# Kernel tuning notes

Measured on AMD Instinct MI355X. Metric: run time of the kernel, lower is better.

## Reference

```python
import jax, jax.numpy as jnp
import numpy as np

N = 100_000   # nodes
E = 3_200_000 # edges (avg degree 32)
K = 10        # propagation hops


def setup_inputs() -> dict:
    key = jax.random.key(0)
    ks = jax.random.split(key, 9)
    x = jax.random.normal(ks[0], (N, 1), dtype=jnp.float32)
    edge_index = jax.random.randint(ks[1], (2, E), 0, N, dtype=jnp.int32)
    # MLP params (lin1: 1->32, lin2: 32->64, fc2: 64->1)
    W1 = jax.random.normal(ks[2], (1, 32), dtype=jnp.float32) * 0.5
    b1 = jnp.zeros((32,), dtype=jnp.float32)
    W2 = jax.random.normal(ks[3], (32, 64), dtype=jnp.float32) * (1.0 / np.sqrt(32))
    b2 = jnp.zeros((64,), dtype=jnp.float32)
    # GPR temp coefficients, Init='Random': uniform(-b, b), b=sqrt(3/(K+1)), L1-normalized
    bound = float(np.sqrt(3.0 / (K + 1)))
    temp = jax.random.uniform(ks[4], (K + 1,), dtype=jnp.float32,
                              minval=-bound, maxval=bound)
    temp = temp / jnp.sum(jnp.abs(temp))
    W_fc = jax.random.normal(ks[5], (64, 1), dtype=jnp.float32) * (1.0 / np.sqrt(64))
    b_fc = jnp.zeros((1,), dtype=jnp.float32)
    return {"x": x, "edge_index": edge_index, "W1": W1, "b1": b1,
            "W2": W2, "b2": b2, "temp": temp, "W_fc": W_fc, "b_fc": b_fc}


def reference(x, edge_index, W1, b1, W2, b2, temp, W_fc, b_fc):
    n = x.shape[0]
    # feature MLP
    h = jax.nn.relu(x @ W1 + b1)       # [N, 32]
    h = jax.nn.relu(h @ W2 + b2)       # [N, 64]
    # gcn_norm with self-loops, edge_weight = 1
    loops = jnp.arange(n, dtype=edge_index.dtype)
    row = jnp.concatenate([edge_index[0], loops])  # source
    col = jnp.concatenate([edge_index[1], loops])  # target (aggregation index)
    ones = jnp.ones(row.shape, dtype=h.dtype)
    deg = jax.ops.segment_sum(ones, col, num_segments=n)
    dinv = jnp.where(deg > 0, jax.lax.rsqrt(deg), 0.0)
    norm = dinv[row] * dinv[col]       # [E+N]
    # K-hop GPR propagation: hidden = sum_k temp[k] * A_hat^k h
    hidden0 = temp[0] * h

    def step(carry, gamma):
        xc, hid = carry
        msg = norm[:, None] * xc[row]                       # gather + scale
        xn = jax.ops.segment_sum(msg, col, num_segments=n)  # scatter-add
        return (xn, hid + gamma * xn), None

    (_, hidden), _ = jax.lax.scan(step, (h, hidden0), temp[1:])
    return hidden @ W_fc + b_fc        # [N, 1]
```

## Files before the change

kernel.cpp:

```cpp
#include <hip/hip_runtime.h>


#define TPB  256
#define SBSH 10
#define CAP1 34304
#define EPT  16
#define CH   (TPB * EPT)

__global__ void k_zero(int* __restrict__ bcursor, int nsb) {
    int i = blockIdx.x * blockDim.x + threadIdx.x;
    if (i < nsb) bcursor[i] = 0;
}

__global__ void k_scatter(const int* __restrict__ erow, const int* __restrict__ ecol,
                          int* __restrict__ bcursor, unsigned int* __restrict__ ebuf1,
                          int e, int nsb) {
    __shared__ int hist[128];
    __shared__ int base[128];
    int t = threadIdx.x;
    int s = blockIdx.x * CH;
    int r[EPT], c[EPT];

    if (t < 128) hist[t] = 0;
    __syncthreads();
#pragma unroll
    for (int j = 0; j < EPT; j++) {
        int i = s + j * TPB + t;
        bool ok = (i < e);
        c[j] = ok ? ecol[i] : -1;
        r[j] = ok ? erow[i] : 0;
        if (ok) atomicAdd(&hist[c[j] >> SBSH], 1);
    }
    __syncthreads();
    if (t < nsb) {
        int cc = hist[t];
        base[t] = cc ? atomicAdd(&bcursor[t], cc) : 0;
        hist[t] = 0;
    }
    __syncthreads();
#pragma unroll
    for (int j = 0; j < EPT; j++) {
        if (c[j] >= 0) {
            int b = c[j] >> SBSH;
            int pos = base[b] + atomicAdd(&hist[b], 1);
            if (pos < CAP1)
                ebuf1[(size_t)b * CAP1 + pos] =
                    ((unsigned int)r[j] << SBSH) | (unsigned int)(c[j] & ((1 << SBSH) - 1));
        }
    }
}

__global__ void __launch_bounds__(1024)
k_sub(const int* __restrict__ bcursor, const unsigned int* __restrict__ ebuf1,
      unsigned int* __restrict__ csr, int2* __restrict__ rs_re,
      float* __restrict__ dinv, float2* __restrict__ nrm, int n) {
    __shared__ int hist[1024];
    __shared__ int wsum[16];
    int b = blockIdx.x;
    int t = threadIdx.x;
    int lane = t & 63;
    int w = t >> 6;

    hist[t] = 0;
    __syncthreads();
    int cnt = min(bcursor[b], CAP1);
    size_t g = (size_t)b * CAP1;
    int last = cnt > 0 ? cnt - 1 : 0;
    for (int j = t; j < cnt; j += 4096) {
        int j1 = j + 1024, j2 = j + 2048, j3 = j + 3072;
        unsigned int p0 = ebuf1[g + j];
        unsigned int p1 = ebuf1[g + min(j1, last)];
        unsigned int p2 = ebuf1[g + min(j2, last)];
        unsigned int p3 = ebuf1[g + min(j3, last)];
        atomicAdd(&hist[p0 & 1023], 1);
        if (j1 < cnt) atomicAdd(&hist[p1 & 1023], 1);
        if (j2 < cnt) atomicAdd(&hist[p2 & 1023], 1);
        if (j3 < cnt) atomicAdd(&hist[p3 & 1023], 1);
    }
    __syncthreads();

    int deg = hist[t];
    int v = deg;
#pragma unroll
    for (int o = 1; o < 64; o <<= 1) {
        int u = __shfl_up(v, o);
        if (lane >= o) v += u;
    }
    if (lane == 63) wsum[w] = v;
    __syncthreads();
    if (w == 0) {
        int sv = (lane < 16) ? wsum[lane] : 0;
#pragma unroll
        for (int o = 1; o < 16; o <<= 1) {
            int u = __shfl_up(sv, o);
            if (lane >= o) sv += u;
        }
        if (lane < 16) wsum[lane] = sv;
    }
    __syncthreads();
    int excl = v - deg + (w > 0 ? wsum[w - 1] : 0);

    int node = (b << SBSH) + t;
    if (node < n) {
        int base = (int)g + excl;
        rs_re[node] = make_int2(base, base + deg);
        float d = (float)(deg + 1);
        float di = rsqrtf(d);
        dinv[node] = di;
        nrm[node] = make_float2(di * di, d * di);
    }
    __syncthreads();
    hist[t] = excl;
    __syncthreads();
    for (int j = t; j < cnt; j += 4096) {
        int j1 = j + 1024, j2 = j + 2048, j3 = j + 3072;
        unsigned int p0 = ebuf1[g + j];
        unsigned int p1 = ebuf1[g + min(j1, last)];
        unsigned int p2 = ebuf1[g + min(j2, last)];
        unsigned int p3 = ebuf1[g + min(j3, last)];
        int pos0 = atomicAdd(&hist[p0 & 1023], 1);
        csr[g + pos0] = p0 >> SBSH;
        if (j1 < cnt) { int pos = atomicAdd(&hist[p1 & 1023], 1); csr[g + pos] = p1 >> SBSH; }
        if (j2 < cnt) { int pos = atomicAdd(&hist[p2 & 1023], 1); csr[g + pos] = p2 >> SBSH; }
        if (j3 < cnt) { int pos = atomicAdd(&hist[p3 & 1023], 1); csr[g + pos] = p3 >> SBSH; }
    }
}

__global__ void k_mlp_z(const float* __restrict__ x, const float* __restrict__ W1,
                        const float* __restrict__ b1, const float* __restrict__ W2,
                        const float* __restrict__ b2, const float* __restrict__ Wfc,
                        const float* __restrict__ bfc, const float* __restrict__ temp,
                        const float* __restrict__ dinv,
                        float* __restrict__ u0, float* __restrict__ out, int n) {
    int wid = (blockIdx.x * blockDim.x + threadIdx.x) >> 6;
    int lane = threadIdx.x & 63;
    if (wid >= n) return;
    float xv = x[wid];
    float acc = b2[lane];
#pragma unroll
    for (int j = 0; j < 32; j++) {
        float h1 = fmaxf(fmaf(xv, W1[j], b1[j]), 0.f);
        acc = fmaf(h1, W2[j * 64 + lane], acc);
    }
    float h2 = fmaxf(acc, 0.f);
    float c = h2 * Wfc[lane];
#pragma unroll
    for (int o = 32; o >= 1; o >>= 1) c += __shfl_xor(c, o);
    if (lane == 0) {
        u0[wid] = dinv[wid] * c;
        out[wid] = fmaf(temp[0], c, bfc[0]);
    }
}

__global__ void k_hop(const int2* __restrict__ rs_re, const unsigned int* __restrict__ csr,
                      const float2* __restrict__ nrm,
                      const float* __restrict__ uprev, float* __restrict__ ucur,
                      float* __restrict__ out, const float* __restrict__ temp,
                      int k, int n, int is_last) {
    int tid = blockIdx.x * blockDim.x + threadIdx.x;
    int node = tid >> 3;
    int sub = tid & 7;
    if (node >= n) return;
    int2 se = rs_re[node];
    int s = se.x, e = se.y;
    float sum = (sub == 0) ? uprev[node] : 0.f;
    for (int i = s + sub; i < e; i += 32) {
        int j1 = i + 8, j2 = i + 16, j3 = i + 24;
        unsigned int a0 = csr[i];
        unsigned int a1 = (j1 < e) ? csr[j1] : 0u;
        unsigned int a2 = (j2 < e) ? csr[j2] : 0u;
        unsigned int a3 = (j3 < e) ? csr[j3] : 0u;
        float v0 = uprev[a0];
        float v1 = uprev[a1];
        float v2 = uprev[a2];
        float v3 = uprev[a3];
        v1 = (j1 < e) ? v1 : 0.f;
        v2 = (j2 < e) ? v2 : 0.f;
        v3 = (j3 < e) ? v3 : 0.f;
        sum += (v0 + v1) + (v2 + v3);
    }
    sum += __shfl_xor(sum, 1);
    sum += __shfl_xor(sum, 2);
    sum += __shfl_xor(sum, 4);
    if (sub == 0) {
        float2 nv = nrm[node];
        float u = nv.x * sum;
        if (!is_last) ucur[node] = u;
        out[node] = fmaf(temp[k] * nv.y, u, out[node]);
    }
}

static inline size_t align256(size_t x) { return (x + 255) & ~(size_t)255; }

extern "C" void kernel_launch(void* const* d_in, const int* in_sizes, int n_in,
                              void* d_out, int out_size, void* d_ws, size_t ws_size,
                              hipStream_t stream) {
    const float* x    = (const float*)d_in[0];
    const int*   ei   = (const int*)d_in[1];
    const float* W1   = (const float*)d_in[2];
    const float* b1   = (const float*)d_in[3];
    const float* W2   = (const float*)d_in[4];
    const float* b2   = (const float*)d_in[5];
    const float* temp = (const float*)d_in[6];
    const float* Wfc  = (const float*)d_in[7];
    const float* bfc  = (const float*)d_in[8];

    const int n = in_sizes[0];
    const int e = in_sizes[1] / 2;
    const int K = in_sizes[6] - 1;
    const int nsb = (n + (1 << SBSH) - 1) >> SBSH;

    const int* erow = ei;
    const int* ecol = ei + e;

    float* out = (float*)d_out;

    char* ws = (char*)d_ws;
    int*          bcursor = (int*)ws;          ws += align256((size_t)128 * 4);
    unsigned int* ebuf1   = (unsigned int*)ws; ws += align256((size_t)nsb * CAP1 * 4);
    unsigned int* csr     = (unsigned int*)ws; ws += align256((size_t)nsb * CAP1 * 4);
    int2*         rs_re   = (int2*)ws;         ws += align256((size_t)n * 8);
    float2*       nrm     = (float2*)ws;       ws += align256((size_t)n * 8);
    float*        dinv    = (float*)ws;        ws += align256((size_t)n * 4);
    float*        u0      = (float*)ws;        ws += align256((size_t)n * 4);
    float*        u1      = (float*)ws;        ws += align256((size_t)n * 4);

    const int gS = (e + CH - 1) / CH;
    const int gW = (n + 3) / 4;
    const int gH = (8 * n + TPB - 1) / TPB;

    k_zero<<<1, 128, 0, stream>>>(bcursor, nsb);
    k_scatter<<<gS, TPB, 0, stream>>>(erow, ecol, bcursor, ebuf1, e, nsb);
    k_sub<<<nsb, 1024, 0, stream>>>(bcursor, ebuf1, csr, rs_re, dinv, nrm, n);
    k_mlp_z<<<gW, 256, 0, stream>>>(x, W1, b1, W2, b2, Wfc, bfc, temp, dinv, u0, out, n);

    float* uin = u0;
    float* uout = u1;
    for (int k = 1; k <= K; k++) {
        k_hop<<<gH, TPB, 0, stream>>>(rs_re, csr, nrm, uin, uout, out, temp,
                                      k, n, (k == K) ? 1 : 0);
        float* t2 = uin; uin = uout; uout = t2;
    }
}
```

Baseline: 341.0 us.

## Pad CSR rows to multiples of four for uint4 gathers and fold MLP into scatter

Each node's CSR segment is padded to a multiple of four entries. The padding slots point to a dummy zero slot at index n, so the hop kernel can load neighbour indices as uint4 without bounds checks. Separately, the MLP is fused into the scatter kernel as a grid-stride loop writing z, and the u0/out initialisation moves into k_sub, which removes one launch. The padding raises per-bucket capacity and adds memory traffic for the padded edges, and the fused MLP adds work to the scatter kernel.

```diff
diff --git a/kernel.cpp b/kernel.cpp
--- a/kernel.cpp
+++ b/kernel.cpp
@@ -3,7 +3,7 @@
 
 #define TPB  256
 #define SBSH 10
-#define CAP1 34304
+#define CAP1 37376
 #define EPT  16
 #define CH   (TPB * EPT)
 
@@ -14,7 +14,10 @@
 
 __global__ void k_scatter(const int* __restrict__ erow, const int* __restrict__ ecol,
                           int* __restrict__ bcursor, unsigned int* __restrict__ ebuf1,
-                          int e, int nsb) {
+                          const float* __restrict__ x, const float* __restrict__ W1,
+                          const float* __restrict__ b1, const float* __restrict__ W2,
+                          const float* __restrict__ b2, const float* __restrict__ Wfc,
+                          float* __restrict__ zarr, int e, int n, int nsb) {
     __shared__ int hist[128];
     __shared__ int base[128];
     int t = threadIdx.x;
@@ -48,12 +51,34 @@
                     ((unsigned int)r[j] << SBSH) | (unsigned int)(c[j] & ((1 << SBSH) - 1));
         }
     }
+
+    int gw = (blockIdx.x * TPB + t) >> 6;
+    int nwaves = (gridDim.x * TPB) >> 6;
+    int lane = t & 63;
+    float b2l = b2[lane];
+    float wfl = Wfc[lane];
+    for (int node = gw; node < n; node += nwaves) {
+        float xv = x[node];
+        float acc = b2l;
+#pragma unroll
+        for (int j = 0; j < 32; j++) {
+            float h1 = fmaxf(fmaf(xv, W1[j], b1[j]), 0.f);
+            acc = fmaf(h1, W2[j * 64 + lane], acc);
+        }
+        float cz = fmaxf(acc, 0.f) * wfl;
+#pragma unroll
+        for (int o = 32; o >= 1; o >>= 1) cz += __shfl_xor(cz, o);
+        if (lane == 0) zarr[node] = cz;
+    }
 }
 
 __global__ void __launch_bounds__(1024)
 k_sub(const int* __restrict__ bcursor, const unsigned int* __restrict__ ebuf1,
       unsigned int* __restrict__ csr, int2* __restrict__ rs_re,
-      float* __restrict__ dinv, float2* __restrict__ nrm, int n) {
+      float2* __restrict__ nrm, const float* __restrict__ zarr,
+      const float* __restrict__ temp, const float* __restrict__ bfc,
+      float* __restrict__ u0, float* __restrict__ u1,
+      float* __restrict__ out, int n) {
     __shared__ int hist[1024];
     __shared__ int wsum[16];
     int b = blockIdx.x;
@@ -80,7 +105,8 @@
     __syncthreads();
 
     int deg = hist[t];
-    int v = deg;
+    int pdeg = (deg + 3) & ~3;
+    int v = pdeg;
 #pragma unroll
     for (int o = 1; o < 64; o <<= 1) {
         int u = __shfl_up(v, o);
@@ -98,19 +124,22 @@
         if (lane < 16) wsum[lane] = sv;
     }
     __syncthreads();
-    int excl = v - deg + (w > 0 ? wsum[w - 1] : 0);
+    int pexcl = v - pdeg + (w > 0 ? wsum[w - 1] : 0);
 
     int node = (b << SBSH) + t;
     if (node < n) {
-        int base = (int)g + excl;
-        rs_re[node] = make_int2(base, base + deg);
+        int bs = (int)g + pexcl;
+        rs_re[node] = make_int2(bs, bs + pdeg);
         float d = (float)(deg + 1);
         float di = rsqrtf(d);
-        dinv[node] = di;
         nrm[node] = make_float2(di * di, d * di);
-    }
-    __syncthreads();
-    hist[t] = excl;
+        float z = zarr[node];
+        u0[node] = di * z;
+        out[node] = fmaf(temp[0], z, bfc[0]);
+    }
+    if (b == 0 && t == 0) { u0[n] = 0.f; u1[n] = 0.f; }
+    __syncthreads();
+    hist[t] = pexcl;
     __syncthreads();
     for (int j = t; j < cnt; j += 4096) {
         int j1 = j + 1024, j2 = j + 2048, j3 = j + 3072;
@@ -120,39 +149,16 @@
         unsigned int p3 = ebuf1[g + min(j3, last)];
         int pos0 = atomicAdd(&hist[p0 & 1023], 1);
         csr[g + pos0] = p0 >> SBSH;
-        if (j1 < cnt) { int pos = atomicAdd(&hist[p1 & 1023], 1); csr[g + pos] = p1 >> SBSH; }
-        if (j2 < cnt) { int pos = atomicAdd(&hist[p2 & 1023], 1); csr[g + pos] = p2 >> SBSH; }
-        if (j3 < cnt) { int pos = atomicAdd(&hist[p3 & 1023], 1); csr[g + pos] = p3 >> SBSH; }
-    }
-}
-
-__global__ void k_mlp_z(const float* __restrict__ x, const float* __restrict__ W1,
-                        const float* __restrict__ b1, const float* __restrict__ W2,
-                        const float* __restrict__ b2, const float* __restrict__ Wfc,
-                        const float* __restrict__ bfc, const float* __restrict__ temp,
-                        const float* __restrict__ dinv,
-                        float* __restrict__ u0, float* __restrict__ out, int n) {
-    int wid = (blockIdx.x * blockDim.x + threadIdx.x) >> 6;
-    int lane = threadIdx.x & 63;
-    if (wid >= n) return;
-    float xv = x[wid];
-    float acc = b2[lane];
-#pragma unroll
-    for (int j = 0; j < 32; j++) {
-        float h1 = fmaxf(fmaf(xv, W1[j], b1[j]), 0.f);
-        acc = fmaf(h1, W2[j * 64 + lane], acc);
-    }
-    float h2 = fmaxf(acc, 0.f);
-    float c = h2 * Wfc[lane];
-#pragma unroll
-    for (int o = 32; o >= 1; o >>= 1) c += __shfl_xor(c, o);
-    if (lane == 0) {
-        u0[wid] = dinv[wid] * c;
-        out[wid] = fmaf(temp[0], c, bfc[0]);
-    }
-}
-
-__global__ void k_hop(const int2* __restrict__ rs_re, const unsigned int* __restrict__ csr,
+        if (j1 < cnt) { int p = atomicAdd(&hist[p1 & 1023], 1); csr[g + p] = p1 >> SBSH; }
+        if (j2 < cnt) { int p = atomicAdd(&hist[p2 & 1023], 1); csr[g + p] = p2 >> SBSH; }
+        if (j3 < cnt) { int p = atomicAdd(&hist[p3 & 1023], 1); csr[g + p] = p3 >> SBSH; }
+    }
+    __syncthreads();
+    for (int p = pexcl + deg; p < pexcl + pdeg; p++)
+        csr[g + p] = (unsigned int)n;
+}
+
+__global__ void k_hop(const int2* __restrict__ rs_re, const uint4* __restrict__ csr4,
                       const float2* __restrict__ nrm,
                       const float* __restrict__ uprev, float* __restrict__ ucur,
                       float* __restrict__ out, const float* __restrict__ temp,
@@ -162,21 +168,15 @@
     int sub = tid & 7;
     if (node >= n) return;
     int2 se = rs_re[node];
-    int s = se.x, e = se.y;
+    int s4 = se.x >> 2;
+    int e4 = se.y >> 2;
     float sum = (sub == 0) ? uprev[node] : 0.f;
-    for (int i = s + sub; i < e; i += 32) {
-        int j1 = i + 8, j2 = i + 16, j3 = i + 24;
-        unsigned int a0 = csr[i];
-        unsigned int a1 = (j1 < e) ? csr[j1] : 0u;
-        unsigned int a2 = (j2 < e) ? csr[j2] : 0u;
-        unsigned int a3 = (j3 < e) ? csr[j3] : 0u;
-        float v0 = uprev[a0];
-        float v1 = uprev[a1];
-        float v2 = uprev[a2];
-        float v3 = uprev[a3];
-        v1 = (j1 < e) ? v1 : 0.f;
-        v2 = (j2 < e) ? v2 : 0.f;
-        v3 = (j3 < e) ? v3 : 0.f;
+    for (int i4 = s4 + sub; i4 < e4; i4 += 8) {
+        uint4 a = csr4[i4];
+        float v0 = uprev[a.x];
+        float v1 = uprev[a.y];
+        float v2 = uprev[a.z];
+        float v3 = uprev[a.w];
         sum += (v0 + v1) + (v2 + v3);
     }
     sum += __shfl_xor(sum, 1);
@@ -190,7 +190,7 @@
     }
 }
 
-static inline size_t align256(size_t x) { return (x + 255) & ~(size_t)255; }
+static inline size_t align256(size_t v) { return (v + 255) & ~(size_t)255; }
 
 extern "C" void kernel_launch(void* const* d_in, const int* in_sizes, int n_in,
                               void* d_out, int out_size, void* d_ws, size_t ws_size,
@@ -221,24 +221,24 @@
     unsigned int* csr     = (unsigned int*)ws; ws += align256((size_t)nsb * CAP1 * 4);
     int2*         rs_re   = (int2*)ws;         ws += align256((size_t)n * 8);
     float2*       nrm     = (float2*)ws;       ws += align256((size_t)n * 8);
-    float*        dinv    = (float*)ws;        ws += align256((size_t)n * 4);
-    float*        u0      = (float*)ws;        ws += align256((size_t)n * 4);
-    float*        u1      = (float*)ws;        ws += align256((size_t)n * 4);
+    float*        zarr    = (float*)ws;        ws += align256((size_t)(n + 1) * 4);
+    float*        u0      = (float*)ws;        ws += align256((size_t)(n + 1) * 4);
+    float*        u1      = (float*)ws;        ws += align256((size_t)(n + 1) * 4);
 
     const int gS = (e + CH - 1) / CH;
-    const int gW = (n + 3) / 4;
     const int gH = (8 * n + TPB - 1) / TPB;
 
     k_zero<<<1, 128, 0, stream>>>(bcursor, nsb);
-    k_scatter<<<gS, TPB, 0, stream>>>(erow, ecol, bcursor, ebuf1, e, nsb);
-    k_sub<<<nsb, 1024, 0, stream>>>(bcursor, ebuf1, csr, rs_re, dinv, nrm, n);
-    k_mlp_z<<<gW, 256, 0, stream>>>(x, W1, b1, W2, b2, Wfc, bfc, temp, dinv, u0, out, n);
+    k_scatter<<<gS, TPB, 0, stream>>>(erow, ecol, bcursor, ebuf1,
+                                      x, W1, b1, W2, b2, Wfc, zarr, e, n, nsb);
+    k_sub<<<nsb, 1024, 0, stream>>>(bcursor, ebuf1, csr, rs_re, nrm,
+                                    zarr, temp, bfc, u0, u1, out, n);
 
     float* uin = u0;
     float* uout = u1;
     for (int k = 1; k <= K; k++) {
-        k_hop<<<gH, TPB, 0, stream>>>(rs_re, csr, nrm, uin, uout, out, temp,
-                                      k, n, (k == K) ? 1 : 0);
+        k_hop<<<gH, TPB, 0, stream>>>(rs_re, (const uint4*)csr, nrm, uin, uout,
+                                      out, temp, k, n, (k == K) ? 1 : 0);
         float* t2 = uin; uin = uout; uout = t2;
     }
 }
```

After: 334.6 us. No clear change (-1.9%).
